# Kernel optimization log

Measured on AMD Instinct MI355X. Metric: run time of the kernel, lower is better.

The kernel has to match this reference:

```python
import jax, jax.numpy as jnp
import numpy as np

B, T, H, L = 64, 512, 768, 9

def setup_inputs() -> dict:
    key = jax.random.key(0)
    ks = jax.random.split(key, 6)
    hidden = jax.random.normal(ks[0], (B, T, H), jnp.float32)
    W = jax.random.normal(ks[1], (H, L), jnp.float32) * 0.02
    b = jnp.zeros((L,), jnp.float32)
    transitions = jax.random.normal(ks[2], (L, L), jnp.float32) * 0.1
    tags = jax.random.randint(ks[3], (B, T), 0, L)
    lengths = jax.random.randint(ks[4], (B,), 1, T + 1)
    return {"hidden": hidden, "W": W, "b": b, "transitions": transitions,
            "tags": tags, "lengths": lengths}


def _crf_log_likelihood(logits, tags, lengths, transitions):
    # logits [B,T,L], tags [B,T] int, lengths [B] int
    Bq, Tq, Lq = logits.shape
    t_idx = jnp.arange(Tq)
    mask = (t_idx[None, :] < lengths[:, None]).astype(logits.dtype)  # [B,T]
    # unary (emission) score along gold path
    unary = jnp.take_along_axis(logits, tags[..., None], axis=2)[..., 0]  # [B,T]
    unary_score = jnp.sum(unary * mask, axis=1)
    # transition score between consecutive gold tags
    trans_gold = transitions[tags[:, :-1], tags[:, 1:]]  # [B,T-1]
    binary_score = jnp.sum(trans_gold * mask[:, 1:], axis=1)
    # log partition via forward algorithm (scan over time)
    def step(alpha, xs):
        logit_t, m_t = xs  # [B,L], [B]
        new = jax.nn.logsumexp(alpha[:, :, None] + transitions[None], axis=1) + logit_t
        alpha = jnp.where(m_t[:, None] > 0, new, alpha)  # carry past seq end
        return alpha, None
    xs = (jnp.swapaxes(logits[:, 1:], 0, 1), jnp.swapaxes(mask[:, 1:], 0, 1))
    alpha, _ = jax.lax.scan(step, logits[:, 0], xs)
    log_norm = jax.nn.logsumexp(alpha, axis=1)
    return unary_score + binary_score - log_norm  # [B]


def _crf_decode(logits, transitions, lengths):
    Bq, Tq, Lq = logits.shape
    t_idx = jnp.arange(Tq)
    mask = t_idx[None, :] < lengths[:, None]  # [B,T] bool
    ident = jnp.broadcast_to(jnp.arange(Lq)[None, :], (Bq, Lq))
    def fwd(state, xs):
        logit_t, m_t = xs  # [B,L], [B]
        scores = state[:, :, None] + transitions[None]  # [B,Lprev,Lcur]
        bp = jnp.argmax(scores, axis=1)                 # [B,L] backpointers
        new = jnp.max(scores, axis=1) + logit_t
        state = jnp.where(m_t[:, None], new, state)
        bp = jnp.where(m_t[:, None], bp, ident)  # pass-through past seq end
        return state, bp
    xs = (jnp.swapaxes(logits[:, 1:], 0, 1), jnp.swapaxes(mask[:, 1:], 0, 1))
    state, bps = jax.lax.scan(fwd, logits[:, 0], xs)  # bps: [T-1,B,L]
    viterbi_score = jnp.max(state, axis=1)  # [B]
    last_tag = jnp.argmax(state, axis=1)    # [B]
    def back(tag, bp):
        prev = jnp.take_along_axis(bp, tag[:, None], axis=1)[:, 0]
        return prev, tag
    first_tag, rev_tags = jax.lax.scan(back, last_tag, bps, reverse=True)
    decode = jnp.concatenate([first_tag[None], rev_tags], axis=0)  # [T,B]
    decode = jnp.swapaxes(decode, 0, 1)
    decode = jnp.where(mask, decode, 0)
    return decode, viterbi_score


def reference(hidden, W, b, transitions, tags, lengths):
    # Dense(label_size, activation='relu') on BERT sequence output
    logits = jax.nn.relu(jnp.einsum('bth,hl->btl', hidden, W) + b)  # [B,T,L]
    ll = _crf_log_likelihood(logits, tags, lengths, transitions)
    loss = -jnp.mean(ll)
    decode, _score = _crf_decode(logits, transitions, lengths)
    return loss, decode
```

## Files before the change

kernel.cpp:

```cpp
#include <hip/hip_runtime.h>
#include <hip/hip_bf16.h>

#define BB 64
#define TT 512
#define HH 768
#define LL 9
#define TS 516

#define LOG2E 1.44269504088896340736f
#define LN2   0.69314718055994530942f

#if __has_builtin(__builtin_amdgcn_logf)
#define LOG2F(x) __builtin_amdgcn_logf(x)
#else
#define LOG2F(x) __log2f(x)
#endif

__device__ __forceinline__ float rlane(float v, int i) {
    return __uint_as_float((unsigned)__builtin_amdgcn_readlane((int)__float_as_uint(v), i));
}

template<int I>
__device__ __forceinline__ float dppb(float v) {
    return __uint_as_float((unsigned)__builtin_amdgcn_mov_dpp(
        (int)__float_as_uint(v), 0x150 + I, 0xF, 0xF, false));
}

__global__ __launch_bounds__(256) void logits_kernel(
    const float* __restrict__ hidden,
    const float* __restrict__ W,
    const float* __restrict__ bias,
    float* __restrict__ logits)
{
    __shared__ __align__(16) float WT[LL][HH];
    __shared__ float bsh[LL];

    const int tid = threadIdx.x;
    for (int idx = tid; idx < HH * LL; idx += 256) {
        int k = idx / LL, l = idx % LL;
        WT[l][k] = W[idx];
    }
    if (tid < LL) bsh[tid] = bias[tid];
    __syncthreads();

    const int wave = tid >> 6;
    const int lane = tid & 63;
    const long base_row = (long)blockIdx.x * 16 + wave * 4;
    const float* hrow = hidden + base_row * HH;

    float acc[4][LL];
#pragma unroll
    for (int r = 0; r < 4; ++r)
#pragma unroll
        for (int l = 0; l < LL; ++l) acc[r][l] = 0.f;

#pragma unroll
    for (int it = 0; it < 3; ++it) {
        const int k = it * 256 + lane * 4;
        float4 h[4];
#pragma unroll
        for (int r = 0; r < 4; ++r)
            h[r] = *(const float4*)(hrow + (long)r * HH + k);
#pragma unroll
        for (int l = 0; l < LL; ++l) {
            float4 w4 = *(const float4*)(&WT[l][k]);
#pragma unroll
            for (int r = 0; r < 4; ++r) {
                acc[r][l] += h[r].x * w4.x + h[r].y * w4.y
                           + h[r].z * w4.z + h[r].w * w4.w;
            }
        }
    }

#pragma unroll
    for (int r = 0; r < 4; ++r)
#pragma unroll
        for (int l = 0; l < LL; ++l) {
            float v = acc[r][l];
#pragma unroll
            for (int off = 32; off; off >>= 1) v += __shfl_xor(v, off, 64);
            acc[r][l] = v;
        }

    if (lane < LL) {
#pragma unroll
        for (int r = 0; r < 4; ++r) {
            float v = acc[r][0];
#pragma unroll
            for (int l = 1; l < LL; ++l) v = (lane == l) ? acc[r][l] : v;
            v += bsh[lane];
            v = v > 0.f ? v : 0.f;
            logits[(base_row + r) * LL + lane] = v;
        }
    }
}

__global__ __launch_bounds__(128) void crf_kernel(
    const float* __restrict__ logits,
    const float* __restrict__ trans,
    const int*  __restrict__ tags,
    const int*  __restrict__ lengths,
    float* __restrict__ ll,
    float* __restrict__ out_decode)
{
    const int b    = blockIdx.x;
    const int tid  = threadIdx.x;
    const int wave = tid >> 6;
    const int lane = tid & 63;

    __shared__ __align__(16) float lgT[LL][TS];
    __shared__ __align__(16) int   tg[TT];
    __shared__ float trS[LL * LL];
    __shared__ __align__(16) float trST[LL][12];
    __shared__ __align__(16) float alphaS[TT][12];
    __shared__ float score_parts[4];

    const int len = lengths[b];
    const float* lgg = logits + (size_t)b * TT * LL;
    for (int i = tid; i < (TT * LL) / 4; i += 128) {
        float4 v = ((const float4*)lgg)[i];
        int base = 4 * i;
        lgT[(base    ) % LL][(base    ) / LL] = v.x;
        lgT[(base + 1) % LL][(base + 1) / LL] = v.y;
        lgT[(base + 2) % LL][(base + 2) / LL] = v.z;
        lgT[(base + 3) % LL][(base + 3) / LL] = v.w;
    }
    {
        const int4* src = (const int4*)(tags + (size_t)b * TT);
        int4* dst = (int4*)tg;
        for (int i = tid; i < TT / 4; i += 128) dst[i] = src[i];
    }
    for (int idx = tid; idx < LL * LL; idx += 128) {
        trS[idx] = trans[idx];
        trST[idx % LL][idx / LL] = trans[idx];
    }
    __syncthreads();

    float u = 0.f, bs = 0.f;
    for (int t = tid; t < len; t += 128) u += lgT[tg[t]][t];
    for (int t = tid + 1; t < len; t += 128) bs += trS[tg[t - 1] * LL + tg[t]];
#pragma unroll
    for (int off = 32; off; off >>= 1) {
        u  += __shfl_xor(u, off, 64);
        bs += __shfl_xor(bs, off, 64);
    }
    if (lane == 0) { score_parts[wave * 2] = u; score_parts[wave * 2 + 1] = bs; }
    __syncthreads();

    const int j = (lane < LL) ? lane : (LL - 1);
    float trc[LL];
#pragma unroll
    for (int i = 0; i < LL; ++i) trc[i] = trS[i * LL + j];

    const float* rowj = &lgT[j][0];

    if (wave == 0) {
        float E0 = exp2f(trc[0] * LOG2E), E1 = exp2f(trc[1] * LOG2E);
        float E2 = exp2f(trc[2] * LOG2E), E3 = exp2f(trc[3] * LOG2E);
        float E4 = exp2f(trc[4] * LOG2E), E5 = exp2f(trc[5] * LOG2E);
        float E6 = exp2f(trc[6] * LOG2E), E7 = exp2f(trc[7] * LOG2E);
        float E8 = exp2f(trc[8] * LOG2E);

        float Mlog = 0.f;
        float P0, P1, P2, P3, P4, P5, P6, P7, P8;
        {
            float Pme = exp2f(rowj[0] * LOG2E);
            P0 = rlane(Pme, 0); P1 = rlane(Pme, 1); P2 = rlane(Pme, 2);
            P3 = rlane(Pme, 3); P4 = rlane(Pme, 4); P5 = rlane(Pme, 5);
            P6 = rlane(Pme, 6); P7 = rlane(Pme, 7); P8 = rlane(Pme, 8);
        }

#define LSTEPL(GV)                                                           \
        { float p0 = P0 * E0, p1 = P1 * E1, p2 = P2 * E2;                    \
          float p3 = P3 * E3, p4 = P4 * E4, p5 = P5 * E5;                    \
          float p6 = P6 * E6, p7 = P7 * E7, p8 = P8 * E8;                    \
          float S = (((p0 + p1) + (p2 + p3)) + ((p4 + p5) + (p6 + p7)))      \
                    + p8;                                                    \
          float Pn = S * (GV);                                               \
          P0 = rlane(Pn, 0); P1 = rlane(Pn, 1); P2 = rlane(Pn, 2);           \
          P3 = rlane(Pn, 3); P4 = rlane(Pn, 4); P5 = rlane(Pn, 5);           \
          P6 = rlane(Pn, 6); P7 = rlane(Pn, 7); P8 = rlane(Pn, 8); }

#define RENORM                                                               \
        { float mx = fmaxf(fmaxf(fmaxf(fmaxf(P0, P1), fmaxf(P2, P3)),       \
                                 fmaxf(fmaxf(P4, P5), fmaxf(P6, P7))), P8); \
          int ex = (int)((__float_as_uint(mx) >> 23) & 255u) - 127;         \
          float sc = __uint_as_float((unsigned)(127 - ex) << 23);           \
          P0 *= sc; P1 *= sc; P2 *= sc; P3 *= sc; P4 *= sc;                 \
          P5 *= sc; P6 *= sc; P7 *= sc; P8 *= sc;                           \
          Mlog += (float)ex; }

        int cb = 8;
        if (len >= 8) {
            float4 c0 = *(const float4*)(rowj);
            float4 c1 = *(const float4*)(rowj + 4);
            float g1 = exp2f(c0.y * LOG2E), g2 = exp2f(c0.z * LOG2E);
            float g3 = exp2f(c0.w * LOG2E), g4 = exp2f(c1.x * LOG2E);
            float g5 = exp2f(c1.y * LOG2E), g6 = exp2f(c1.z * LOG2E);
            float g7 = exp2f(c1.w * LOG2E);
            LSTEPL(g1) LSTEPL(g2) LSTEPL(g3)
            LSTEPL(g4) LSTEPL(g5) LSTEPL(g6) LSTEPL(g7)

            float4 n0 = *(const float4*)(rowj + 8);
            float4 n1 = *(const float4*)(rowj + 12);
            for (; cb + 8 <= len; cb += 8) {
                float4 c0b = n0; float4 c1b = n1;
                if (cb + 8 < TT) {
                    n0 = *(const float4*)(rowj + cb + 8);
                    n1 = *(const float4*)(rowj + cb + 12);
                }
                float g0 = exp2f(c0b.x * LOG2E), g1b = exp2f(c0b.y * LOG2E);
                float g2b = exp2f(c0b.z * LOG2E), g3b = exp2f(c0b.w * LOG2E);
                float g4b = exp2f(c1b.x * LOG2E), g5b = exp2f(c1b.y * LOG2E);
                float g6b = exp2f(c1b.z * LOG2E), g7b = exp2f(c1b.w * LOG2E);
                RENORM
                LSTEPL(g0)  LSTEPL(g1b) LSTEPL(g2b) LSTEPL(g3b)
                LSTEPL(g4b) LSTEPL(g5b) LSTEPL(g6b) LSTEPL(g7b)
            }
        } else {
            cb = 1;
        }
        for (int t = cb; t < len; ++t) {
            float g = exp2f(rowj[t] * LOG2E);
            LSTEPL(g)
        }
        {
            float S = (((P0 + P1) + (P2 + P3)) + ((P4 + P5) + (P6 + P7)))
                      + P8;
            float log_norm = (Mlog + LOG2F(S)) * LN2;
            if (lane == 0) {
                float unary  = score_parts[0] + score_parts[2];
                float binary = score_parts[1] + score_parts[3];
                ll[b] = unary + binary - log_norm;
            }
        }
    } else {
        const int acol = (lane < LL) ? lane : 11;
        float a0, a1, a2, a3, a4, a5, a6, a7, a8;
        {
            float lg0 = rowj[0];
            alphaS[0][acol] = lg0;
            a0 = dppb<0>(lg0); a1 = dppb<1>(lg0); a2 = dppb<2>(lg0);
            a3 = dppb<3>(lg0); a4 = dppb<4>(lg0); a5 = dppb<5>(lg0);
            a6 = dppb<6>(lg0); a7 = dppb<7>(lg0); a8 = dppb<8>(lg0);
        }

#define VSTEP3(LGV, TVAL)                                                    \
        { float s0 = a0 + trc[0], s1 = a1 + trc[1];                          \
          float s2 = a2 + trc[2], s3 = a3 + trc[3];                          \
          float s4 = a4 + trc[4], s5 = a5 + trc[5];                          \
          float s6 = a6 + trc[6], s7 = a7 + trc[7];                          \
          float s8 = a8 + trc[8];                                            \
          float m012 = fmaxf(fmaxf(s0, s1), s2);                             \
          float m345 = fmaxf(fmaxf(s3, s4), s5);                             \
          float m678 = fmaxf(fmaxf(s6, s7), s8);                             \
          float bv   = fmaxf(fmaxf(m012, m345), m678);                       \
          float ns = bv + (LGV);                                             \
          alphaS[TVAL][acol] = ns;                                           \
          a0 = dppb<0>(ns); a1 = dppb<1>(ns); a2 = dppb<2>(ns);              \
          a3 = dppb<3>(ns); a4 = dppb<4>(ns); a5 = dppb<5>(ns);              \
          a6 = dppb<6>(ns); a7 = dppb<7>(ns); a8 = dppb<8>(ns); }

        int cb = 8;
        if (len >= 8) {
            float4 c0 = *(const float4*)(rowj);
            float4 c1 = *(const float4*)(rowj + 4);
            VSTEP3(c0.y, 1) VSTEP3(c0.z, 2) VSTEP3(c0.w, 3)
            VSTEP3(c1.x, 4) VSTEP3(c1.y, 5) VSTEP3(c1.z, 6) VSTEP3(c1.w, 7)

            float4 n0 = *(const float4*)(rowj + 8);
            float4 n1 = *(const float4*)(rowj + 12);
            for (; cb + 8 <= len; cb += 8) {
                float4 c0b = n0; float4 c1b = n1;
                if (cb + 8 < TT) {
                    n0 = *(const float4*)(rowj + cb + 8);
                    n1 = *(const float4*)(rowj + cb + 12);
                }
                VSTEP3(c0b.x, cb + 0) VSTEP3(c0b.y, cb + 1)
                VSTEP3(c0b.z, cb + 2) VSTEP3(c0b.w, cb + 3)
                VSTEP3(c1b.x, cb + 4) VSTEP3(c1b.y, cb + 5)
                VSTEP3(c1b.z, cb + 6) VSTEP3(c1b.w, cb + 7)
            }
        } else {
            cb = 1;
        }
        for (int t = cb; t < len; ++t) {
            float lgv = rowj[t];
            VSTEP3(lgv, t)
        }

        int last_tag;
        {
            float m012 = fmaxf(fmaxf(a0, a1), a2);
            float m345 = fmaxf(fmaxf(a3, a4), a5);
            float m678 = fmaxf(fmaxf(a6, a7), a8);
            float bv   = fmaxf(fmaxf(m012, m345), m678);
            int bi = 8;
            bi = (a7 == bv) ? 7 : bi;
            bi = (a6 == bv) ? 6 : bi;
            bi = (a5 == bv) ? 5 : bi;
            bi = (a4 == bv) ? 4 : bi;
            bi = (a3 == bv) ? 3 : bi;
            bi = (a2 == bv) ? 2 : bi;
            bi = (a1 == bv) ? 1 : bi;
            bi = (a0 == bv) ? 0 : bi;
            last_tag = __builtin_amdgcn_readfirstlane(bi);
        }

        const unsigned long long IDENT = 0x876543210ULL;
        unsigned long long f[8];
        const int t0 = lane * 8;
#pragma unroll
        for (int m2 = 0; m2 < 8; ++m2) {
            int t = t0 + m2;
            unsigned long long F = IDENT;
            if (t >= 1 && t < len) {
                float4 A0 = *(const float4*)&alphaS[t - 1][0];
                float4 A1 = *(const float4*)&alphaS[t - 1][4];
                float  A8 = alphaS[t - 1][8];
                F = 0ULL;
#pragma unroll
                for (int jj = 0; jj < LL; ++jj) {
                    float4 T0 = *(const float4*)&trST[jj][0];
                    float4 T1 = *(const float4*)&trST[jj][4];
                    float  T8 = trST[jj][8];
                    float s0 = A0.x + T0.x, s1 = A0.y + T0.y;
                    float s2 = A0.z + T0.z, s3 = A0.w + T0.w;
                    float s4 = A1.x + T1.x, s5 = A1.y + T1.y;
                    float s6 = A1.z + T1.z, s7 = A1.w + T1.w;
                    float s8 = A8 + T8;
                    float m012 = fmaxf(fmaxf(s0, s1), s2);
                    float m345 = fmaxf(fmaxf(s3, s4), s5);
                    float m678 = fmaxf(fmaxf(s6, s7), s8);
                    float bv   = fmaxf(fmaxf(m012, m345), m678);
                    int bi = 8;
                    bi = (s7 == bv) ? 7 : bi;
                    bi = (s6 == bv) ? 6 : bi;
                    bi = (s5 == bv) ? 5 : bi;
                    bi = (s4 == bv) ? 4 : bi;
                    bi = (s3 == bv) ? 3 : bi;
                    bi = (s2 == bv) ? 2 : bi;
                    bi = (s1 == bv) ? 1 : bi;
                    bi = (s0 == bv) ? 0 : bi;
                    F |= ((unsigned long long)bi) << (4 * jj);
                }
            }
            f[m2] = F;
        }

        unsigned long long h = f[7];
#pragma unroll
        for (int m2 = 6; m2 >= 0; --m2) {
            unsigned long long hn = 0ULL;
#pragma unroll
            for (int jj = 0; jj < LL; ++jj) {
                int v = (int)((h >> (4 * jj)) & 15ULL);
                int w = (int)((f[m2] >> (4 * v)) & 15ULL);
                hn |= ((unsigned long long)w) << (4 * jj);
            }
            h = hn;
        }
        const unsigned hlo = (unsigned)h, hhi = (unsigned)(h >> 32);
        int tag = last_tag;
        int entry = last_tag;
        for (int l2 = 63; l2 >= 0; --l2) {
            unsigned glo = (unsigned)__builtin_amdgcn_readlane((int)hlo, l2);
            unsigned ghi = (unsigned)__builtin_amdgcn_readlane((int)hhi, l2);
            unsigned long long g = ((unsigned long long)ghi << 32) | glo;
            if (l2 == lane) entry = tag;
            tag = (int)((g >> (4 * tag)) & 15ULL);
        }
        float* dec = out_decode + (size_t)b * TT;
        int e = entry;
        {
            int t = t0 + 7;
            dec[t] = (t < len) ? (float)e : 0.f;
        }
#pragma unroll
        for (int m2 = 7; m2 >= 1; --m2) {
            e = (int)((f[m2] >> (4 * e)) & 15ULL);
            int t = t0 + m2 - 1;
            dec[t] = (t < len) ? (float)e : 0.f;
        }
    }
}

__global__ __launch_bounds__(64) void loss_kernel(const float* __restrict__ ll,
                                                  float* __restrict__ out)
{
    const int lane = threadIdx.x;
    float v = ll[lane];
#pragma unroll
    for (int off = 32; off; off >>= 1) v += __shfl_xor(v, off, 64);
    if (lane == 0) out[0] = -v * (1.0f / 64.0f);
}

extern "C" void kernel_launch(void* const* d_in, const int* in_sizes, int n_in,
                              void* d_out, int out_size, void* d_ws, size_t ws_size,
                              hipStream_t stream)
{
    const float* hidden  = (const float*)d_in[0];
    const float* W       = (const float*)d_in[1];
    const float* bias    = (const float*)d_in[2];
    const float* trans   = (const float*)d_in[3];
    const int*   tags    = (const int*)d_in[4];
    const int*   lengths = (const int*)d_in[5];

    float* out = (float*)d_out;
    float* logits = (float*)d_ws;
    float* ll     = logits + (size_t)BB * TT * LL;

    logits_kernel<<<2048, 256, 0, stream>>>(hidden, W, bias, logits);
    crf_kernel<<<BB, 128, 0, stream>>>(logits, trans, tags, lengths, ll, out + 1);
    loss_kernel<<<1, 64, 0, stream>>>(ll, out);
}
```

Before: 78.53 us.

## Fuse loss reduction into CRF kernel and remap logits GEMV to row groups

Removes the separate loss kernel launch. The last CRF block, detected through an atomic counter that the logits kernel resets, now sums the per-sequence log-likelihoods. Separately, the logits kernel maps each 16-lane group to one row instead of having each wave reduce four rows across all 64 lanes. This shortens the shuffle reduction from six to four steps and cuts the accumulator registers. The price is a serialized 64-element sum inside one thread and a more complex cross-block ordering via atomics and fences.

```diff
diff --git a/kernel.cpp b/kernel.cpp
--- a/kernel.cpp
+++ b/kernel.cpp
@@ -30,8 +30,11 @@
     const float* __restrict__ hidden,
     const float* __restrict__ W,
     const float* __restrict__ bias,
-    float* __restrict__ logits)
+    float* __restrict__ logits,
+    int* __restrict__ ctr)
 {
+    if (blockIdx.x == 0 && threadIdx.x == 0) atomicExch(ctr, 0);
+
     __shared__ __align__(16) float WT[LL][HH];
     __shared__ float bsh[LL];
 
@@ -45,53 +48,41 @@
 
     const int wave = tid >> 6;
     const int lane = tid & 63;
-    const long base_row = (long)blockIdx.x * 16 + wave * 4;
-    const float* hrow = hidden + base_row * HH;
-
-    float acc[4][LL];
-#pragma unroll
-    for (int r = 0; r < 4; ++r)
-#pragma unroll
-        for (int l = 0; l < LL; ++l) acc[r][l] = 0.f;
-
-#pragma unroll
-    for (int it = 0; it < 3; ++it) {
-        const int k = it * 256 + lane * 4;
-        float4 h[4];
-#pragma unroll
-        for (int r = 0; r < 4; ++r)
-            h[r] = *(const float4*)(hrow + (long)r * HH + k);
+    const int grp  = lane >> 4;
+    const int sl   = lane & 15;
+    const long row = (long)blockIdx.x * 16 + wave * 4 + grp;
+    const float* hrow = hidden + row * HH;
+
+    float acc[LL];
+#pragma unroll
+    for (int l = 0; l < LL; ++l) acc[l] = 0.f;
+
+#pragma unroll
+    for (int it = 0; it < 12; ++it) {
+        const int k = it * 64 + sl * 4;
+        float4 h = *(const float4*)(hrow + k);
 #pragma unroll
         for (int l = 0; l < LL; ++l) {
             float4 w4 = *(const float4*)(&WT[l][k]);
-#pragma unroll
-            for (int r = 0; r < 4; ++r) {
-                acc[r][l] += h[r].x * w4.x + h[r].y * w4.y
-                           + h[r].z * w4.z + h[r].w * w4.w;
-            }
-        }
-    }
-
-#pragma unroll
-    for (int r = 0; r < 4; ++r)
-#pragma unroll
-        for (int l = 0; l < LL; ++l) {
-            float v = acc[r][l];
-#pragma unroll
-            for (int off = 32; off; off >>= 1) v += __shfl_xor(v, off, 64);
-            acc[r][l] = v;
-        }
-
-    if (lane < LL) {
-#pragma unroll
-        for (int r = 0; r < 4; ++r) {
-            float v = acc[r][0];
-#pragma unroll
-            for (int l = 1; l < LL; ++l) v = (lane == l) ? acc[r][l] : v;
-            v += bsh[lane];
-            v = v > 0.f ? v : 0.f;
-            logits[(base_row + r) * LL + lane] = v;
-        }
+            acc[l] += h.x * w4.x + h.y * w4.y + h.z * w4.z + h.w * w4.w;
+        }
+    }
+
+#pragma unroll
+    for (int l = 0; l < LL; ++l) {
+        float v = acc[l];
+#pragma unroll
+        for (int off = 8; off; off >>= 1) v += __shfl_xor(v, off, 64);
+        acc[l] = v;
+    }
+
+    if (sl < LL) {
+        float v = acc[0];
+#pragma unroll
+        for (int l = 1; l < LL; ++l) v = (sl == l) ? acc[l] : v;
+        v += bsh[sl];
+        v = v > 0.f ? v : 0.f;
+        logits[row * LL + sl] = v;
     }
 }
 
@@ -101,7 +92,9 @@
     const int*  __restrict__ tags,
     const int*  __restrict__ lengths,
     float* __restrict__ ll,
-    float* __restrict__ out_decode)
+    float* __restrict__ out_loss,
+    float* __restrict__ out_decode,
+    int* __restrict__ ctr)
 {
     const int b    = blockIdx.x;
     const int tid  = threadIdx.x;
@@ -232,6 +225,16 @@
                 float unary  = score_parts[0] + score_parts[2];
                 float binary = score_parts[1] + score_parts[3];
                 ll[b] = unary + binary - log_norm;
+
+                __threadfence();
+                int old = atomicAdd(ctr, 1);
+                if (old == BB - 1) {
+                    __threadfence();
+                    float s = 0.f;
+                    const volatile float* llv = (const volatile float*)ll;
+                    for (int i = 0; i < BB; ++i) s += llv[i];
+                    out_loss[0] = -s * (1.0f / 64.0f);
+                }
             }
         }
     } else {
@@ -385,16 +388,6 @@
     }
 }
 
-__global__ __launch_bounds__(64) void loss_kernel(const float* __restrict__ ll,
-                                                  float* __restrict__ out)
-{
-    const int lane = threadIdx.x;
-    float v = ll[lane];
-#pragma unroll
-    for (int off = 32; off; off >>= 1) v += __shfl_xor(v, off, 64);
-    if (lane == 0) out[0] = -v * (1.0f / 64.0f);
-}
-
 extern "C" void kernel_launch(void* const* d_in, const int* in_sizes, int n_in,
                               void* d_out, int out_size, void* d_ws, size_t ws_size,
                               hipStream_t stream)
@@ -409,8 +402,9 @@
     float* out = (float*)d_out;
     float* logits = (float*)d_ws;
     float* ll     = logits + (size_t)BB * TT * LL;
-
-    logits_kernel<<<2048, 256, 0, stream>>>(hidden, W, bias, logits);
-    crf_kernel<<<BB, 128, 0, stream>>>(logits, trans, tags, lengths, ll, out + 1);
-    loss_kernel<<<1, 64, 0, stream>>>(ll, out);
+    int*   ctr    = (int*)(ll + 64);
+
+    logits_kernel<<<2048, 256, 0, stream>>>(hidden, W, bias, logits, ctr);
+    crf_kernel<<<BB, 128, 0, stream>>>(logits, trans, tags, lengths, ll,
+                                       out, out + 1, ctr);
 }
```

After: 67.48 us. -14.1%, faster.
